# Kernel optimization log

Measured on AMD Instinct MI355X. Metric: run time of the kernel, lower is better.

Reference implementation:

```python
import jax, jax.numpy as jnp
import numpy as np

B_, L_, D_ = 2, 4096, 1024
E_ = 2
DI = E_ * D_            # 2048
H_ = 16
HD_ = DI // H_          # 128
N_ = 128
K_ = 4                  # d_conv
CS_ = 256               # SSD chunk size
MC_ = 256               # Hebbian memory chunk size
ALPHA = 0.5             # memory_alpha (== write_alpha default)


def _silu(x):
    return x * jax.nn.sigmoid(x)


def _rmsnorm(x, w, eps=1e-6):
    return x * jax.lax.rsqrt(jnp.mean(x * x, axis=-1, keepdims=True) + eps) * w


def setup_inputs() -> dict:
    key = jax.random.key(0)
    ks = jax.random.split(key, 8)
    proj_dim = 2 * DI + 2 * H_ * N_ + H_
    n = lambda k, sh, sc: jax.random.normal(k, sh, jnp.float32) * sc
    return {
        "x": n(ks[0], (B_, L_, D_), 1.0),
        "norm_w": jnp.ones((D_,), jnp.float32),
        "w_in": n(ks[1], (proj_dim, D_), 0.02),
        "conv_w": n(ks[2], (DI, K_), 0.2),
        "conv_b": jnp.zeros((DI,), jnp.float32),
        "A_log": jnp.log(2.0 * jnp.ones((H_,), jnp.float32)),
        "dt_bias": jnp.zeros((H_,), jnp.float32),
        "D_skip": jnp.ones((DI,), jnp.float32),
        "w_out": n(ks[3], (D_, DI), 0.02),
        "w_write": n(ks[4], (D_, D_), 0.02),
        "w_read": n(ks[5], (D_, D_), 0.02),
        "decay": jnp.float32(4.6),
    }


def _forward(x, norm_w, w_in, conv_w, conv_b, A_log, dt_bias, D_skip,
             w_out, w_write, w_read, decay):
    B, L, D = x.shape
    residual = x
    xn = _rmsnorm(x, norm_w)

    # ---- SSDBlock ----
    proj = xn @ w_in.T  # (B,L,2*DI+2*H*N+H)
    val = proj[..., :DI]
    gate = proj[..., DI:2 * DI]
    Bp = proj[..., 2 * DI:2 * DI + H_ * N_].reshape(B, L, H_, N_)
    Cp = proj[..., 2 * DI + H_ * N_:2 * DI + 2 * H_ * N_].reshape(B, L, H_, N_)
    dt = jax.nn.softplus(proj[..., -H_:] + dt_bias)  # (B,L,H)

    # causal depthwise conv1d (kernel K_, groups=DI)
    vp = jnp.pad(val, ((0, 0), (K_ - 1, 0), (0, 0)))
    val = sum(conv_w[:, k] * vp[:, k:k + L, :] for k in range(K_)) + conv_b
    val = _silu(val).reshape(B, L, H_, HD_)

    ld = dt * (-jnp.exp(A_log))  # log decay (B,L,H)

    nc = L // CS_
    to_chunks = lambda a: jnp.moveaxis(a.reshape(B, nc, CS_, *a.shape[2:]), 1, 0)
    tril = jnp.tril(jnp.ones((CS_, CS_), bool))
    Dv = D_skip.reshape(1, H_, 1, HD_)

    def ssd_chunk(h, inp):
        v_c, b_c, c_c, ld_c = inp  # (B,CS,H,HD), (B,CS,H,N), (B,CS,H,N), (B,CS,H)
        cum = jnp.cumsum(ld_c, axis=1)            # (B,CS,H)
        cum_h = jnp.transpose(cum, (0, 2, 1))     # (B,H,CS)
        dd = cum_h[:, :, :, None] - cum_h[:, :, None, :]
        Lmat = jnp.where(tril, jnp.exp(dd), 0.0)
        M = jnp.einsum('blhn,bmhn->bhlm', c_c, b_c) * Lmat
        v_h = jnp.transpose(v_c, (0, 2, 1, 3))    # (B,H,CS,HD)
        Y = M @ v_h
        Y = Y + jnp.einsum('blhn,bhdn,blh->bhld', c_c, h, jnp.exp(cum))
        Y = Y + Dv * v_h
        h = jnp.exp(cum[:, -1])[:, :, None, None] * h + \
            jnp.einsum('blhd,blhn,blh->bhdn', v_c, b_c, jnp.exp(cum[:, -1:, :] - cum))
        return h, Y

    h0 = jnp.zeros((B, H_, HD_, N_), jnp.float32)
    _, Ys = jax.lax.scan(ssd_chunk, h0,
                         (to_chunks(val), to_chunks(Bp), to_chunks(Cp), to_chunks(ld)))
    # (nc,B,H,CS,HD) -> (B,L,DI)
    Y = jnp.transpose(Ys, (1, 0, 3, 2, 4)).reshape(B, L, DI)
    out = (Y * _silu(gate)) @ w_out.T  # (B,L,D)

    # ---- Hebbian memory (chunkwise) ----
    gamma = jax.nn.sigmoid(decay)
    lg = jnp.log(gamma)
    v = out @ w_write.T
    wk = jnp.pad(out[:, :-1], ((0, 0), (1, 0), (0, 0)))  # shifted write keys
    p = jnp.arange(MC_)
    diffs = jnp.maximum(p[:, None] - 1 - p[None, :], 0).astype(jnp.float32)
    causal = (p[:, None] > p[None, :]).astype(jnp.float32)
    Mmem = jnp.exp(diffs * lg) * causal
    gp = gamma ** p                    # read decay by position in chunk
    gw = gamma ** (MC_ - 1 - p)        # write decay to end of chunk
    nm = L // MC_
    tom = lambda a: jnp.moveaxis(a.reshape(B, nm, MC_, D), 1, 0)

    def mem_chunk(W, inp):
        rk_c, wk_c, v_c = inp  # (B,MC,D)
        inter = jnp.einsum('bde,bte->btd', W, rk_c) * gp[None, :, None]
        S = jnp.einsum('bie,bje->bij', rk_c, wk_c)
        intra = (S * Mmem) @ v_c
        W = gamma ** MC_ * W + jnp.einsum('btd,bte->bde', v_c * gw[None, :, None], wk_c)
        return W, inter + intra

    W0 = jnp.zeros((B, D, D), jnp.float32)
    _, reads = jax.lax.scan(mem_chunk, W0, (tom(out), tom(wk), tom(v)))
    reads = jnp.moveaxis(reads, 0, 1).reshape(B, L, D)
    out = out + ALPHA * (reads @ w_read.T)
    return residual + out


def reference(x, norm_w, w_in, conv_w, conv_b, A_log, dt_bias, D_skip,
              w_out, w_write, w_read, decay):
    return _forward(x, norm_w, w_in, conv_w, conv_b, A_log, dt_bias, D_skip,
                    w_out, w_write, w_read, decay)
```

## Files before the change

kernel.cpp:

```cpp
#include <hip/hip_runtime.h>
#include <hip/hip_bf16.h>

typedef __hip_bfloat16 bf16;
typedef __attribute__((ext_vector_type(8))) short short8;
typedef __attribute__((ext_vector_type(4))) float floatx4;
typedef __attribute__((ext_vector_type(16))) float floatx16;

#define B_ 2
#define L_ 4096
#define D_ 1024
#define DI_ 2048
#define H_ 16
#define HD_ 128
#define N_ 128
#define CS_ 256
#define MC_ 256
#define NC_ 16
#define PROJ_ 8208

__device__ __forceinline__ float bf2f(short s) {
    return __uint_as_float(((unsigned)(unsigned short)s) << 16);
}
__device__ __forceinline__ short f2bf(float f) {
    __hip_bfloat16 h = __float2bfloat16(f);
    return *(short*)&h;
}

__device__ __forceinline__ void gl_lds16(const void* g, void* s) {
    __builtin_amdgcn_global_load_lds(
        (const __attribute__((address_space(1))) void*)g,
        (__attribute__((address_space(3))) void*)s, 16, 0, 0);
}

struct GemmP {
    const bf16* A; const bf16* Bt;
    float* C; bf16* CB; bf16* CB2; bf16* CB3;
    const float* add0; const float* add1; const bf16* add0b; const float* scr;
    long lda, ldb, ldc;
    int M, N, K, zinner, tri;
    long a_zo, a_zi, b_zo, b_zi, c_zo, c_zi;
};

template<int EPI>
__global__ __launch_bounds__(256, 2) void gemm_bt(GemmP p)
{
    int NT = gridDim.x, MT = gridDim.y;
    long T = (long)NT * MT * gridDim.z;
    long flat = ((long)blockIdx.z * MT + blockIdx.y) * NT + blockIdx.x;
    int xcd = (int)(flat & 7);
    long q = flat >> 3;
    long Tq = T >> 3; int Tr = (int)(T & 7);
    long tile = (long)xcd * Tq + (long)(xcd < Tr ? xcd : Tr) + q;
    long per_z = (long)NT * MT;
    int z = (int)(tile / per_z);
    int t2 = (int)(tile - (long)z * per_z);
    int FG = NT >> 3;
    int g, width, within;
    if (t2 < FG * MT * 8) { g = t2 / (MT * 8); width = 8; within = t2 - g * MT * 8; }
    else                  { g = FG; width = NT - FG * 8; within = t2 - FG * MT * 8; }
    int m_outer = within / (8 * width);
    int hb = MT - m_outer * 8; if (hb > 8) hb = 8;
    int inner = within - m_outer * 8 * width;
    int n_in = inner / hb, m_in = inner - n_in * hb;
    int m0 = (m_outer * 8 + m_in) * 128;
    int n0 = (g * 8 + n_in) * 128;

    int zo = z / p.zinner, zi = z % p.zinner;
    const bf16* A  = p.A  + (long)zo * p.a_zo + (long)zi * p.a_zi;
    const bf16* Bt = p.Bt + (long)zo * p.b_zo + (long)zi * p.b_zi;
    long coff = (long)zo * p.c_zo + (long)zi * p.c_zi;

    int tid = threadIdx.x;
    int lane = tid & 63, wave = tid >> 6;
    int wm = (wave >> 1) * 64, wn = (wave & 1) * 64;
    int ln31 = lane & 31, hi = lane >> 5;

    if (p.tri == 1 && n0 >= m0 + 128) {
        if (EPI == 3) {
#pragma unroll
            for (int i = 0; i < 2; i++)
#pragma unroll
                for (int j = 0; j < 2; j++)
#pragma unroll
                    for (int r = 0; r < 16; r++) {
                        int gm = m0 + wm + i * 32 + (r & 3) + 8 * (r >> 2) + 4 * hi;
                        int gn = n0 + wn + j * 32 + ln31;
                        if (gm < p.M && gn < p.N)
                            p.CB[coff + (long)gm * p.ldc + gn] = __float2bfloat16(0.f);
                    }
        }
        return;
    }
    int Keff = (p.tri == 2) ? (m0 + 128 < p.K ? m0 + 128 : p.K) : p.K;

    __shared__ __align__(16) bf16 As[128 * 64];
    __shared__ __align__(16) bf16 Bs[128 * 64];

    floatx16 acc[2][2];
#pragma unroll
    for (int i = 0; i < 2; i++)
#pragma unroll
        for (int j = 0; j < 2; j++)
#pragma unroll
            for (int r = 0; r < 16; r++) acc[i][j][r] = 0.f;

    int lrow = lane >> 3;
    int lc = ((lane & 7) ^ lrow) * 8;
    int wrow = wave * 32;
    int rx = lane & 7;

    for (int k0 = 0; k0 < Keff; k0 += 64) {
#pragma unroll
        for (int t = 0; t < 4; t++) {
            int row = wrow + t * 8 + lrow;
            gl_lds16(A + (long)(m0 + row) * p.lda + k0 + lc, &As[(wrow + t * 8) * 64]);
            int bn = n0 + row; if (bn > p.N - 1) bn = p.N - 1;
            gl_lds16(Bt + (long)bn * p.ldb + k0 + lc, &Bs[(wrow + t * 8) * 64]);
        }
        __syncthreads();
#pragma unroll
        for (int ks = 0; ks < 64; ks += 16) {
            int lb = (ks >> 3) + hi;
            int po = ((lb ^ rx) << 3);
            short8 af[2], bq[2];
#pragma unroll
            for (int i = 0; i < 2; i++)
                af[i] = *(const short8*)&As[(wm + i * 32 + ln31) * 64 + po];
#pragma unroll
            for (int j = 0; j < 2; j++)
                bq[j] = *(const short8*)&Bs[(wn + j * 32 + ln31) * 64 + po];
#pragma unroll
            for (int i = 0; i < 2; i++)
#pragma unroll
                for (int j = 0; j < 2; j++)
                    acc[i][j] = __builtin_amdgcn_mfma_f32_32x32x16_bf16(af[i], bq[j], acc[i][j], 0, 0, 0);
        }
        __syncthreads();
    }

#pragma unroll
    for (int i = 0; i < 2; i++) {
#pragma unroll
        for (int j = 0; j < 2; j++) {
#pragma unroll
            for (int r = 0; r < 16; r++) {
                int gm = m0 + wm + i * 32 + (r & 3) + 8 * (r >> 2) + 4 * hi;
                int gn = n0 + wn + j * 32 + ln31;
                if (gm >= p.M || gn >= p.N) continue;
                float a = acc[i][j][r];
                if (EPI == 0) {
                    p.C[coff + (long)gm * p.ldc + gn] = a;
                } else if (EPI == 2) {
                    if (gn < 2048)      p.CB [(long)gm * 2048 + gn]          = __float2bfloat16(a);
                    else if (gn < 4096) p.CB2[(long)gm * 2048 + (gn - 2048)] = __float2bfloat16(a);
                    else if (gn < 8192) p.CB3[(long)gm * 4096 + (gn - 4096)] = __float2bfloat16(a);
                    else                p.C  [(long)gm * 16   + (gn - 8192)] = a;
                } else if (EPI == 3) {
                    float lg = p.scr[1];
                    float v = (gm > gn) ? a * __expf((float)(gm - 1 - gn) * lg) : 0.f;
                    p.CB[coff + (long)gm * p.ldc + gn] = __float2bfloat16(v);
                } else if (EPI == 4) {
                    long ix = coff + (long)gm * p.ldc + gn;
                    float t = a * p.scr[16 + gm] + __bfloat162float(p.add0b[ix]);
                    p.CB[ix] = __float2bfloat16(t);
                } else if (EPI == 6) {
                    p.CB[coff + (long)gm * p.ldc + gn] = __float2bfloat16(a);
                } else if (EPI == 7) {
                    long ix = (long)gm * p.ldc + gn;
                    p.C[ix] = p.add0[ix] + __bfloat162float(p.add0b[ix]) + 0.5f * a;
                } else if (EPI == 8) {
                    long ix = (long)gm * p.ldc + gn;
                    bf16 v = __float2bfloat16(a);
                    p.CB[ix] = v;
                    int l = gm & (L_ - 1);
                    if (l != L_ - 1) p.CB2[ix + p.ldc] = v;
                    if (l == 0) p.CB2[ix] = __float2bfloat16(0.f);
                }
            }
        }
    }
}

__global__ void k_gamma(const float* decay, float* scr)
{
    int t = threadIdx.x;
    float g = 1.f / (1.f + expf(-decay[0]));
    float lg = logf(g);
    if (t == 0) { scr[0] = g; scr[1] = lg; scr[2] = expf(256.f * lg); }
    scr[16 + t]  = expf(lg * (float)t);
    scr[272 + t] = expf(lg * (float)(255 - t));
}

__global__ void k_f2ball(const float* __restrict__ s0, bf16* __restrict__ d0, long n0,
                         const float* __restrict__ s1, bf16* __restrict__ d1, long n1,
                         const float* __restrict__ s2, bf16* __restrict__ d2, long n2,
                         const float* __restrict__ s3, bf16* __restrict__ d3, long n3)
{
    long i = (long)blockIdx.x * 256 + threadIdx.x;
    const float* s; bf16* d; long rel = i;
    if (rel < n0) { s = s0; d = d0; }
    else { rel -= n0;
        if (rel < n1) { s = s1; d = d1; }
        else { rel -= n1;
            if (rel < n2) { s = s2; d = d2; }
            else { rel -= n2; if (rel >= n3) return; s = s3; d = d3; }
        }
    }
    float4 v = ((const float4*)s)[rel];
    bf16* o = d + rel * 4;
    o[0] = __float2bfloat16(v.x); o[1] = __float2bfloat16(v.y);
    o[2] = __float2bfloat16(v.z); o[3] = __float2bfloat16(v.w);
}

__global__ __launch_bounds__(256) void k_rmsnorm(const float* __restrict__ x,
                                                 const float* __restrict__ w,
                                                 bf16* __restrict__ o)
{
    int row = blockIdx.x, t = threadIdx.x;
    float4 xv = ((const float4*)(x + (long)row * D_))[t];
    float s = xv.x*xv.x + xv.y*xv.y + xv.z*xv.z + xv.w*xv.w;
#pragma unroll
    for (int m = 32; m > 0; m >>= 1) s += __shfl_xor(s, m, 64);
    __shared__ float ps[4];
    if ((t & 63) == 0) ps[t >> 6] = s;
    __syncthreads();
    s = ps[0] + ps[1] + ps[2] + ps[3];
    float r = rsqrtf(s * (1.f / (float)D_) + 1e-6f);
    float4 wv = ((const float4*)w)[t];
    bf16* orow = o + (long)row * D_ + t * 4;
    orow[0] = __float2bfloat16(xv.x * r * wv.x);
    orow[1] = __float2bfloat16(xv.y * r * wv.y);
    orow[2] = __float2bfloat16(xv.z * r * wv.z);
    orow[3] = __float2bfloat16(xv.w * r * wv.w);
}

__global__ __launch_bounds__(256) void k_cum(const float* __restrict__ dtr,
                                             const float* __restrict__ dt_bias,
                                             const float* __restrict__ A_log,
                                             float* __restrict__ cum_g,
                                             float* __restrict__ cumlast)
{
    int bid = blockIdx.x;
    int h = bid & 15, c = (bid >> 4) & 15, b = bid >> 8;
    long rowbase = (long)b * L_ + c * CS_;
    int tid = threadIdx.x;
    __shared__ float cum_s[256];
    float d = dtr[(rowbase + tid) * H_ + h] + dt_bias[h];
    float sp = (d > 20.f) ? d : log1pf(__expf(d));
    cum_s[tid] = -__expf(A_log[h]) * sp;
    __syncthreads();
    for (int off = 1; off < 256; off <<= 1) {
        float add = (tid >= off) ? cum_s[tid - off] : 0.f;
        __syncthreads();
        cum_s[tid] += add;
        __syncthreads();
    }
    cum_g[(rowbase + tid) * H_ + h] = cum_s[tid];
    if (tid == 255) cumlast[bid] = cum_s[255];
}

__global__ void k_vtc(const bf16* __restrict__ val_b, const float* __restrict__ cw,
                      const float* __restrict__ cb, bf16* __restrict__ vT)
{
    __shared__ bf16 tile[35][33];
    int b = blockIdx.z;
    int r0 = blockIdx.x * 32, c0 = blockIdx.y * 32;
    int tid = threadIdx.x;
    for (int idx = tid; idx < 35 * 32; idx += 256) {
        int row = idx >> 5, ch = idx & 31;
        int gl = r0 - 3 + row;
        bf16 v = __float2bfloat16(0.f);
        if (gl >= 0 && gl < L_) v = val_b[((long)b * L_ + gl) * 2048 + c0 + ch];
        tile[row][ch] = v;
    }
    __syncthreads();
    int tx = tid & 31, ty = tid >> 5;
    int l = r0 + tx;
    for (int i = 0; i < 32; i += 8) {
        int ch = c0 + ty + i;
        float4 cwv = ((const float4*)cw)[ch];
        float acc = cb[ch]
                  + cwv.x * __bfloat162float(tile[tx][ty + i])
                  + cwv.y * __bfloat162float(tile[tx + 1][ty + i])
                  + cwv.z * __bfloat162float(tile[tx + 2][ty + i])
                  + cwv.w * __bfloat162float(tile[tx + 3][ty + i]);
        float s = acc / (1.f + __expf(-acc));
        vT[((long)b * 2048 + ch) * L_ + l] = __float2bfloat16(s);
    }
}

__global__ void k_bt(const bf16* __restrict__ bc, bf16* __restrict__ BT)
{
    __shared__ bf16 tile[32][33];
    int b = blockIdx.z;
    int r0 = blockIdx.x * 32, c0 = blockIdx.y * 32;
    int tx = threadIdx.x & 31, ty = threadIdx.x >> 5;
    for (int i = 0; i < 32; i += 8)
        tile[ty + i][tx] = bc[((long)b * L_ + r0 + ty + i) * 4096 + c0 + tx];
    __syncthreads();
    int l = r0 + tx;
    for (int i = 0; i < 32; i += 8) {
        int col = c0 + ty + i;
        BT[((long)b * 2048 + col) * L_ + l] = tile[tx][ty + i];
    }
}

__global__ __launch_bounds__(256, 2) void k_ssd_u2(
    const bf16* __restrict__ vT, const bf16* __restrict__ BT,
    const float* __restrict__ cum_g, const float* __restrict__ cumlast,
    bf16* __restrict__ U)
{
    int bid = blockIdx.x;
    int h = bid & 15, c = (bid >> 4) & 15, b = bid >> 8;
    long rowbase = (long)b * L_ + c * CS_;
    int tid = threadIdx.x;
    __shared__ float w_s[256];
    w_s[tid] = __expf(cumlast[bid] - cum_g[(rowbase + tid) * H_ + h]);
    __syncthreads();
    int lane = tid & 63, wave = tid >> 6;
    int r16 = lane & 15, q8 = (lane >> 4) * 8, rq = (lane >> 4) * 4;
    int d0 = (wave >> 1) * 64, n0 = (wave & 1) * 64;
    const bf16* vb = vT + ((long)b * 2048 + h * 128) * L_ + c * 256;
    const bf16* bb = BT + ((long)b * 2048 + h * 128) * L_ + c * 256;
    floatx4 zero4 = {0.f, 0.f, 0.f, 0.f};
    floatx4 acc[4][4];
#pragma unroll
    for (int i = 0; i < 4; i++)
#pragma unroll
        for (int j = 0; j < 4; j++) acc[i][j] = zero4;
#pragma unroll 2
    for (int ks = 0; ks < 8; ks++) {
        float wv[8];
#pragma unroll
        for (int j = 0; j < 8; j++) wv[j] = w_s[ks * 32 + q8 + j];
        short8 af[4], bq[4];
#pragma unroll
        for (int i = 0; i < 4; i++) {
            short8 raw = *(const short8*)(vb + (long)(d0 + i * 16 + r16) * L_ + ks * 32 + q8);
#pragma unroll
            for (int j = 0; j < 8; j++) {
                float f = bf2f(raw[j]) * wv[j];
                raw[j] = (short)(__float_as_uint(f) >> 16);
            }
            af[i] = raw;
        }
#pragma unroll
        for (int j = 0; j < 4; j++)
            bq[j] = *(const short8*)(bb + (long)(n0 + j * 16 + r16) * L_ + ks * 32 + q8);
#pragma unroll
        for (int i = 0; i < 4; i++)
#pragma unroll
            for (int j = 0; j < 4; j++)
                acc[i][j] = __builtin_amdgcn_mfma_f32_16x16x32_bf16(af[i], bq[j], acc[i][j], 0, 0, 0);
    }
    bf16* up = U + (((long)c * B_ + b) * H_ + h) * 16384;
#pragma unroll
    for (int i = 0; i < 4; i++)
#pragma unroll
        for (int j = 0; j < 4; j++)
#pragma unroll
            for (int r = 0; r < 4; r++)
                up[(d0 + i * 16 + rq + r) * 128 + (n0 + j * 16 + r16)] = __float2bfloat16(acc[i][j][r]);
}

__global__ void k_ssd2(const bf16* __restrict__ U, const float* __restrict__ cumlast,
                       bf16* __restrict__ hst)
{
    const long tot = (long)B_ * H_ * HD_ * N_;
    long idx = ((long)blockIdx.x * 256 + threadIdx.x) * 8;
    if (idx >= tot) return;
    int bh = (int)(idx >> 14);
    int b = bh >> 4, h = bh & 15;
    float hv[8];
#pragma unroll
    for (int j = 0; j < 8; j++) hv[j] = 0.f;
    for (int c = 0; c < NC_; c++) {
        float ef = __expf(cumlast[b * 256 + c * 16 + h]);
        short8 u = *(const short8*)(U + c * tot + idx);
        short8 o;
#pragma unroll
        for (int j = 0; j < 8; j++) {
            o[j] = f2bf(hv[j]);
            hv[j] = ef * hv[j] + bf2f(u[j]);
        }
        *(short8*)(hst + c * tot + idx) = o;
    }
}

__global__ __launch_bounds__(256, 2) void k_ssd_y(
    const bf16* __restrict__ bc_b, const bf16* __restrict__ vT,
    const bf16* __restrict__ hst, const float* __restrict__ cum_g,
    const float* __restrict__ Dskip, const bf16* __restrict__ gate_b,
    bf16* __restrict__ yg)
{
    int bid = blockIdx.x;
    int h = bid & 15, c = (bid >> 4) & 15, b = bid >> 8;
    long rowbase = (long)b * L_ + c * CS_;
    int tid = threadIdx.x, lane = tid & 63, wave = tid >> 6;
    int r16 = lane & 15, q8 = (lane >> 4) * 8, rq = (lane >> 4) * 4;
    int wt = (wave >> 1) * 32, wmS = (wave & 1) * 32, wd = (wave & 1) * 64;

    __shared__ float cum_s[256];
    __shared__ __align__(16) bf16 Ss[64][72];

    cum_s[tid] = cum_g[(rowbase + tid) * H_ + h];
    __syncthreads();

    const bf16* Cb  = bc_b + rowbase * 4096 + 2048 + h * 128;
    const bf16* Bb  = bc_b + rowbase * 4096 + h * 128;
    const bf16* vTb = vT + ((long)b * 2048 + h * 128) * L_ + c * 256;
    const bf16* hp  = hst + (((long)c * B_ + b) * H_ + h) * 16384;

    floatx4 zero4 = {0.f, 0.f, 0.f, 0.f};

    for (int tt = 0; tt < 4; tt++) {
        int tbase = tt * 64;
        short8 caf[2][4];
#pragma unroll
        for (int i = 0; i < 2; i++)
#pragma unroll
            for (int ks = 0; ks < 4; ks++)
                caf[i][ks] = *(const short8*)(Cb + (long)(tbase + wt + i * 16 + r16) * 4096 + ks * 32 + q8);

        floatx4 yacc[2][4];
#pragma unroll
        for (int i = 0; i < 2; i++)
#pragma unroll
            for (int j = 0; j < 4; j++) yacc[i][j] = zero4;
#pragma unroll
        for (int ks = 0; ks < 4; ks++)
#pragma unroll
            for (int j = 0; j < 4; j++) {
                short8 hq = *(const short8*)(hp + (long)(wd + j * 16 + r16) * 128 + ks * 32 + q8);
#pragma unroll
                for (int i = 0; i < 2; i++)
                    yacc[i][j] = __builtin_amdgcn_mfma_f32_16x16x32_bf16(caf[i][ks], hq, yacc[i][j], 0, 0, 0);
            }
        float texp[2][4];
#pragma unroll
        for (int i = 0; i < 2; i++)
#pragma unroll
            for (int r = 0; r < 4; r++)
                texp[i][r] = __expf(cum_s[tbase + wt + i * 16 + rq + r]);
#pragma unroll
        for (int i = 0; i < 2; i++)
#pragma unroll
            for (int j = 0; j < 4; j++)
#pragma unroll
                for (int r = 0; r < 4; r++) yacc[i][j][r] *= texp[i][r];

        for (int mt = 0; mt <= tt; mt++) {
            int mbase = mt * 64;
            floatx4 sacc[2][2];
#pragma unroll
            for (int i = 0; i < 2; i++)
#pragma unroll
                for (int j = 0; j < 2; j++) sacc[i][j] = zero4;
#pragma unroll
            for (int ks = 0; ks < 4; ks++) {
                short8 bq[2];
#pragma unroll
                for (int j = 0; j < 2; j++)
                    bq[j] = *(const short8*)(Bb + (long)(mbase + wmS + j * 16 + r16) * 4096 + ks * 32 + q8);
#pragma unroll
                for (int i = 0; i < 2; i++)
#pragma unroll
                    for (int j = 0; j < 2; j++)
                        sacc[i][j] = __builtin_amdgcn_mfma_f32_16x16x32_bf16(caf[i][ks], bq[j], sacc[i][j], 0, 0, 0);
            }
            __syncthreads();
#pragma unroll
            for (int i = 0; i < 2; i++)
#pragma unroll
                for (int r = 0; r < 4; r++) {
                    int trow = wt + i * 16 + rq + r;
                    float ct = cum_s[tbase + trow];
#pragma unroll
                    for (int j = 0; j < 2; j++) {
                        int mcol = mbase + wmS + j * 16 + r16;
                        float val = (mcol <= tbase + trow) ? sacc[i][j][r] * __expf(ct - cum_s[mcol]) : 0.f;
                        Ss[trow][wmS + j * 16 + r16] = __float2bfloat16(val);
                    }
                }
            __syncthreads();
#pragma unroll
            for (int ks = 0; ks < 2; ks++) {
                short8 saf[2];
#pragma unroll
                for (int i = 0; i < 2; i++)
                    saf[i] = *(const short8*)&Ss[wt + i * 16 + r16][ks * 32 + q8];
#pragma unroll
                for (int j = 0; j < 4; j++) {
                    short8 vq = *(const short8*)(vTb + (long)(wd + j * 16 + r16) * L_ + mbase + ks * 32 + q8);
#pragma unroll
                    for (int i = 0; i < 2; i++)
                        yacc[i][j] = __builtin_amdgcn_mfma_f32_16x16x32_bf16(saf[i], vq, yacc[i][j], 0, 0, 0);
                }
            }
        }
#pragma unroll
        for (int i = 0; i < 2; i++)
#pragma unroll
            for (int r = 0; r < 4; r++) {
                int t = tbase + wt + i * 16 + rq + r;
                long grow = (rowbase + t) * 2048 + h * 128;
#pragma unroll
                for (int j = 0; j < 4; j++) {
                    int d = wd + j * 16 + r16;
                    float vv = __bfloat162float(vTb[(long)d * L_ + t]);
                    float y = yacc[i][j][r] + Dskip[h * 128 + d] * vv;
                    float g = __bfloat162float(gate_b[grow + d]);
                    float sg = g / (1.f + __expf(-g));
                    yg[grow + d] = __float2bfloat16(y * sg);
                }
            }
    }
}

__global__ void k_trans2(const bf16* __restrict__ vbuf, const bf16* __restrict__ outg,
                         const float* __restrict__ scr,
                         bf16* __restrict__ vTm, bf16* __restrict__ wkgT)
{
    __shared__ bf16 tv[32][33];
    __shared__ bf16 tw[32][33];
    int b = blockIdx.z;
    const bf16* srcv = vbuf + (long)b * L_ * D_;
    const bf16* srco = outg + (long)b * L_ * D_;
    int r0 = blockIdx.x * 32, c0 = blockIdx.y * 32;
    int tx = threadIdx.x & 31, ty = threadIdx.x >> 5;
    for (int i = 0; i < 32; i += 8) {
        int rr = r0 + ty + i;
        tv[ty + i][tx] = srcv[(long)rr * D_ + c0 + tx];
        float g = scr[272 + (rr & 255)];
        float w = (rr == 0) ? 0.f : __bfloat162float(srco[(long)(rr - 1) * D_ + c0 + tx]) * g;
        tw[ty + i][tx] = __float2bfloat16(w);
    }
    __syncthreads();
    bf16* dv = vTm + (long)b * D_ * L_;
    bf16* dw = wkgT + (long)b * D_ * L_;
    for (int i = 0; i < 32; i += 8) {
        long o = (long)(c0 + ty + i) * L_ + r0 + tx;
        dv[o] = tv[tx][ty + i];
        dw[o] = tw[tx][ty + i];
    }
}

__global__ void k_m2(bf16* __restrict__ UwW, const float* __restrict__ scr)
{
    const long tot = (long)B_ * D_ * D_;
    long idx = ((long)blockIdx.x * 256 + threadIdx.x) * 8;
    if (idx >= tot) return;
    float gMC = scr[2];
    float w[8];
#pragma unroll
    for (int j = 0; j < 8; j++) w[j] = 0.f;
    for (int c = 0; c < NC_; c++) {
        short8 u = *(const short8*)(UwW + c * tot + idx);
        short8 o;
#pragma unroll
        for (int j = 0; j < 8; j++) {
            o[j] = f2bf(w[j]);
            w[j] = gMC * w[j] + bf2f(u[j]);
        }
        *(short8*)(UwW + c * tot + idx) = o;
    }
}

static inline int cdiv_i(long a, long b) { return (int)((a + b - 1) / b); }

static void run_gemm(hipStream_t st, int epi, const bf16* A, const bf16* Bt,
                     float* C, bf16* CB, bf16* CB2, bf16* CB3,
                     const float* add0, const float* add1, const bf16* add0b,
                     const float* scr, int M, int N, int K,
                     long lda, long ldb, long ldc, int nbatch, int zinner,
                     long a_zo, long a_zi, long b_zo, long b_zi, long c_zo, long c_zi,
                     int tri = 0)
{
    GemmP p;
    p.A = A; p.Bt = Bt; p.C = C; p.CB = CB; p.CB2 = CB2; p.CB3 = CB3;
    p.add0 = add0; p.add1 = add1; p.add0b = add0b; p.scr = scr;
    p.lda = lda; p.ldb = ldb; p.ldc = ldc;
    p.M = M; p.N = N; p.K = K; p.zinner = zinner; p.tri = tri;
    p.a_zo = a_zo; p.a_zi = a_zi; p.b_zo = b_zo; p.b_zi = b_zi; p.c_zo = c_zo; p.c_zi = c_zi;
    dim3 g(cdiv_i(N, 128), cdiv_i(M, 128), nbatch);
    dim3 b(256);
    switch (epi) {
        case 0: gemm_bt<0><<<g, b, 0, st>>>(p); break;
        case 2: gemm_bt<2><<<g, b, 0, st>>>(p); break;
        case 3: gemm_bt<3><<<g, b, 0, st>>>(p); break;
        case 4: gemm_bt<4><<<g, b, 0, st>>>(p); break;
        case 6: gemm_bt<6><<<g, b, 0, st>>>(p); break;
        case 7: gemm_bt<7><<<g, b, 0, st>>>(p); break;
        case 8: gemm_bt<8><<<g, b, 0, st>>>(p); break;
    }
}

extern "C" void kernel_launch(void* const* d_in, const int* in_sizes, int n_in,
                              void* d_out, int out_size, void* d_ws, size_t ws_size,
                              hipStream_t stream)
{
    const float* x       = (const float*)d_in[0];
    const float* norm_w  = (const float*)d_in[1];
    const float* w_in    = (const float*)d_in[2];
    const float* conv_w  = (const float*)d_in[3];
    const float* conv_b  = (const float*)d_in[4];
    const float* A_log   = (const float*)d_in[5];
    const float* dt_bias = (const float*)d_in[6];
    const float* D_skip  = (const float*)d_in[7];
    const float* w_out   = (const float*)d_in[8];
    const float* w_write = (const float*)d_in[9];
    const float* w_read  = (const float*)d_in[10];
    const float* decay   = (const float*)d_in[11];
    float* outp = (float*)d_out;

    const size_t SZ_SCR  = 4096;
    const size_t SZ_DT   = (size_t)B_ * L_ * H_ * 4;
    const size_t SZ_CUML = 2048;
    const size_t SZ_WOUT = (size_t)D_ * DI_ * 2;
    const size_t SZ_WSML = (size_t)D_ * D_ * 2;
    const size_t SZ_R1   = (size_t)B_ * L_ * 2048 * 2;
    const size_t SZ_R2   = SZ_R1;
    const size_t SZ_R3   = (size_t)B_ * L_ * 4096 * 2;
    const size_t SZ_R4   = (size_t)B_ * L_ * D_ * 2 + (size_t)PROJ_ * D_ * 2;
    const size_t SZ_R5   = (size_t)B_ * L_ * 2048 * 4;

    size_t o = 0;
    auto take = [&](size_t sz) { size_t r = o; o += (sz + 255) & ~(size_t)255; return r; };
    const size_t O_SCR = take(SZ_SCR);
    const size_t O_DT  = take(SZ_DT);
    const size_t O_LD  = take(SZ_DT);
    const size_t O_CUM = take(SZ_DT);
    const size_t O_CL  = take(SZ_CUML);
    const size_t O_WO  = take(SZ_WOUT);
    const size_t O_WW  = take(SZ_WSML);
    const size_t O_WR  = take(SZ_WSML);
    const size_t O_R1  = take(SZ_R1);
    const size_t O_R2  = take(SZ_R2);
    const size_t O_R3  = take(SZ_R3);
    const size_t O_R4  = take(SZ_R4);
    const size_t O_R5  = take(SZ_R5);
    const size_t NEED = o;
    if (ws_size < NEED) return;
    (void)O_LD;

    char* ws = (char*)d_ws;
    float* scr     = (float*)(ws + O_SCR);
    float* dt_raw  = (float*)(ws + O_DT);
    float* cum_g   = (float*)(ws + O_CUM);
    float* cumlast = (float*)(ws + O_CL);
    bf16*  w_out_b   = (bf16*)(ws + O_WO);
    bf16*  w_write_b = (bf16*)(ws + O_WW);
    bf16*  w_read_b  = (bf16*)(ws + O_WR);

    bf16*  val_b   = (bf16*)(ws + O_R1);
    bf16*  yg_b    = (bf16*)(ws + O_R1);
    bf16*  hst_b   = (bf16*)(ws + O_R1 + (size_t)B_ * L_ * D_ * 2);
    bf16*  Sm_b    = (bf16*)(ws + O_R1);
    bf16*  intra_b = (bf16*)(ws + O_R1 + (size_t)NC_ * B_ * MC_ * MC_ * 2);
    bf16*  gate_b  = (bf16*)(ws + O_R2);
    bf16*  out_b   = (bf16*)(ws + O_R2);
    bf16*  wk_b    = (bf16*)(ws + O_R2 + (size_t)B_ * L_ * D_ * 2);
    bf16*  reads_b = wk_b;
    bf16*  bc_b    = (bf16*)(ws + O_R3);
    bf16*  UwW     = (bf16*)(ws + O_R3);
    bf16*  xn_b    = (bf16*)(ws + O_R4);
    bf16*  w_in_b  = (bf16*)(ws + O_R4 + (size_t)B_ * L_ * D_ * 2);
    bf16*  U_ssd   = (bf16*)(ws + O_R4);
    bf16*  vT_g    = (bf16*)(ws + O_R5);
    bf16*  BT_g    = (bf16*)(ws + O_R5 + (size_t)B_ * L_ * 2048 * 2);
    bf16*  vbuf_b  = (bf16*)(ws + O_R5);
    bf16*  vTm     = (bf16*)(ws + O_R5 + (size_t)B_ * L_ * D_ * 4);
    bf16*  wkgT    = (bf16*)(ws + O_R5 + (size_t)B_ * L_ * D_ * 4 + (size_t)B_ * L_ * D_ * 2);

    k_gamma<<<1, 256, 0, stream>>>(decay, scr);
    {
        long n0 = (long)PROJ_ * D_ / 4, n1 = (long)D_ * DI_ / 4;
        long n2 = (long)D_ * D_ / 4,   n3 = n2;
        k_f2ball<<<cdiv_i(n0 + n1 + n2 + n3, 256), 256, 0, stream>>>(
            w_in, w_in_b, n0, w_out, w_out_b, n1, w_write, w_write_b, n2, w_read, w_read_b, n3);
    }
    k_rmsnorm<<<B_ * L_, 256, 0, stream>>>(x, norm_w, xn_b);
    run_gemm(stream, 2, xn_b, w_in_b, dt_raw, val_b, gate_b, bc_b, nullptr, nullptr, nullptr, nullptr,
             B_ * L_, PROJ_, D_, D_, D_, 0, 1, 1, 0, 0, 0, 0, 0, 0);
    k_cum<<<B_ * NC_ * H_, 256, 0, stream>>>(dt_raw, dt_bias, A_log, cum_g, cumlast);
    k_vtc<<<dim3(L_ / 32, DI_ / 32, B_), 256, 0, stream>>>(val_b, conv_w, conv_b, vT_g);
    k_bt<<<dim3(L_ / 32, DI_ / 32, B_), 256, 0, stream>>>(bc_b, BT_g);
    k_ssd_u2<<<B_ * NC_ * H_, 256, 0, stream>>>(vT_g, BT_g, cum_g, cumlast, U_ssd);
    k_ssd2<<<cdiv_i((long)B_ * H_ * HD_ * N_ / 8, 256), 256, 0, stream>>>(U_ssd, cumlast, hst_b);
    k_ssd_y<<<B_ * NC_ * H_, 256, 0, stream>>>(bc_b, vT_g, hst_b, cum_g, D_skip, gate_b, yg_b);
    run_gemm(stream, 8, yg_b, w_out_b, nullptr, out_b, wk_b, nullptr, nullptr, nullptr, nullptr, nullptr,
             B_ * L_, D_, DI_, DI_, DI_, D_, 1, 1, 0, 0, 0, 0, 0, 0);
    run_gemm(stream, 6, out_b, w_write_b, nullptr, vbuf_b, nullptr, nullptr, nullptr, nullptr, nullptr, nullptr,
             B_ * L_, D_, D_, D_, D_, D_, 1, 1, 0, 0, 0, 0, 0, 0);
    k_trans2<<<dim3(L_ / 32, D_ / 32, B_), 256, 0, stream>>>(vbuf_b, out_b, scr, vTm, wkgT);
    run_gemm(stream, 6, vTm, wkgT, nullptr, UwW, nullptr, nullptr, nullptr, nullptr, nullptr, nullptr,
             D_, D_, MC_, L_, L_, D_, B_ * NC_, NC_,
             (long)D_ * L_, MC_, (long)D_ * L_, MC_, (long)D_ * D_, (long)B_ * D_ * D_);
    k_m2<<<cdiv_i((long)B_ * D_ * D_ / 8, 256), 256, 0, stream>>>(UwW, scr);
    run_gemm(stream, 3, out_b, wk_b, nullptr, Sm_b, nullptr, nullptr, nullptr, nullptr, nullptr, scr,
             MC_, MC_, D_, D_, D_, MC_, B_ * NC_, NC_,
             (long)L_ * D_, (long)MC_ * D_, (long)L_ * D_, (long)MC_ * D_,
             (long)MC_ * MC_, (long)B_ * MC_ * MC_, 1);
    run_gemm(stream, 6, Sm_b, vTm, nullptr, intra_b, nullptr, nullptr, nullptr, nullptr, nullptr, nullptr,
             MC_, D_, MC_, MC_, L_, D_, B_ * NC_, NC_,
             (long)MC_ * MC_, (long)B_ * MC_ * MC_, (long)D_ * L_, MC_,
             (long)L_ * D_, (long)MC_ * D_, 2);
    run_gemm(stream, 4, out_b, UwW, nullptr, reads_b, nullptr, nullptr, nullptr, nullptr, intra_b, scr,
             MC_, D_, D_, D_, D_, D_, B_ * NC_, NC_,
             (long)L_ * D_, (long)MC_ * D_, (long)D_ * D_, (long)B_ * D_ * D_,
             (long)L_ * D_, (long)MC_ * D_);
    run_gemm(stream, 7, reads_b, w_read_b, outp, nullptr, nullptr, nullptr, x, nullptr, out_b, nullptr,
             B_ * L_, D_, D_, D_, D_, D_, 1, 1, 0, 0, 0, 0, 0, 0);
}
```

Before: 756.2 us.

## Fuse transposed stores into GEMM epilogues and drop separate transpose kernels

The input-projection GEMM epilogue now stages the accumulator tile in shared memory and writes the val and B projections already transposed (channel-major) to global memory. This removes the k_bt transpose kernel and lets the conv/SiLU kernel become a simple vectorized row pass. The write-projection GEMM likewise emits the transposed value matrix directly through a new epilogue, so the follow-up transpose kernel only has to handle the gated write keys. The cost is an extra LDS round trip and barrier in those epilogues, plus a shared buffer reused between the main loop and the epilogue.

```diff
diff --git a/kernel.cpp b/kernel.cpp
--- a/kernel.cpp
+++ b/kernel.cpp
@@ -34,7 +34,7 @@
 
 struct GemmP {
     const bf16* A; const bf16* Bt;
-    float* C; bf16* CB; bf16* CB2; bf16* CB3;
+    float* C; bf16* CB; bf16* CB2; bf16* CB3; bf16* CB4;
     const float* add0; const float* add1; const bf16* add0b; const float* scr;
     long lda, ldb, ldc;
     int M, N, K, zinner, tri;
@@ -75,6 +75,10 @@
     int wm = (wave >> 1) * 64, wn = (wave & 1) * 64;
     int ln31 = lane & 31, hi = lane >> 5;
 
+    __shared__ __align__(16) bf16 Sh[2 * 128 * 64];
+    bf16* As = Sh;
+    bf16* Bs = Sh + 128 * 64;
+
     if (p.tri == 1 && n0 >= m0 + 128) {
         if (EPI == 3) {
 #pragma unroll
@@ -93,9 +97,6 @@
     }
     int Keff = (p.tri == 2) ? (m0 + 128 < p.K ? m0 + 128 : p.K) : p.K;
 
-    __shared__ __align__(16) bf16 As[128 * 64];
-    __shared__ __align__(16) bf16 Bs[128 * 64];
-
     floatx16 acc[2][2];
 #pragma unroll
     for (int i = 0; i < 2; i++)
@@ -138,44 +139,78 @@
         __syncthreads();
     }
 
-#pragma unroll
-    for (int i = 0; i < 2; i++) {
-#pragma unroll
-        for (int j = 0; j < 2; j++) {
-#pragma unroll
-            for (int r = 0; r < 16; r++) {
-                int gm = m0 + wm + i * 32 + (r & 3) + 8 * (r >> 2) + 4 * hi;
-                int gn = n0 + wn + j * 32 + ln31;
-                if (gm >= p.M || gn >= p.N) continue;
-                float a = acc[i][j][r];
-                if (EPI == 0) {
-                    p.C[coff + (long)gm * p.ldc + gn] = a;
-                } else if (EPI == 2) {
-                    if (gn < 2048)      p.CB [(long)gm * 2048 + gn]          = __float2bfloat16(a);
-                    else if (gn < 4096) p.CB2[(long)gm * 2048 + (gn - 2048)] = __float2bfloat16(a);
-                    else if (gn < 8192) p.CB3[(long)gm * 4096 + (gn - 4096)] = __float2bfloat16(a);
-                    else                p.C  [(long)gm * 16   + (gn - 8192)] = a;
-                } else if (EPI == 3) {
-                    float lg = p.scr[1];
-                    float v = (gm > gn) ? a * __expf((float)(gm - 1 - gn) * lg) : 0.f;
-                    p.CB[coff + (long)gm * p.ldc + gn] = __float2bfloat16(v);
-                } else if (EPI == 4) {
-                    long ix = coff + (long)gm * p.ldc + gn;
-                    float t = a * p.scr[16 + gm] + __bfloat162float(p.add0b[ix]);
-                    p.CB[ix] = __float2bfloat16(t);
-                } else if (EPI == 6) {
-                    p.CB[coff + (long)gm * p.ldc + gn] = __float2bfloat16(a);
-                } else if (EPI == 7) {
-                    long ix = (long)gm * p.ldc + gn;
-                    p.C[ix] = p.add0[ix] + __bfloat162float(p.add0b[ix]) + 0.5f * a;
-                } else if (EPI == 8) {
-                    long ix = (long)gm * p.ldc + gn;
-                    bf16 v = __float2bfloat16(a);
-                    p.CB[ix] = v;
-                    int l = gm & (L_ - 1);
-                    if (l != L_ - 1) p.CB2[ix + p.ldc] = v;
-                    if (l == 0) p.CB2[ix] = __float2bfloat16(0.f);
+    if (EPI != 9) {
+#pragma unroll
+        for (int i = 0; i < 2; i++) {
+#pragma unroll
+            for (int j = 0; j < 2; j++) {
+#pragma unroll
+                for (int r = 0; r < 16; r++) {
+                    int gm = m0 + wm + i * 32 + (r & 3) + 8 * (r >> 2) + 4 * hi;
+                    int gn = n0 + wn + j * 32 + ln31;
+                    if (gm >= p.M || gn >= p.N) continue;
+                    float a = acc[i][j][r];
+                    if (EPI == 0) {
+                        p.C[coff + (long)gm * p.ldc + gn] = a;
+                    } else if (EPI == 2) {
+                        if (gn >= 8192)     p.C  [(long)gm * 16   + (gn - 8192)] = a;
+                        else if (gn >= 4096) p.CB3[(long)gm * 4096 + (gn - 4096)] = __float2bfloat16(a);
+                        else if (gn >= 2048) p.CB2[(long)gm * 2048 + (gn - 2048)] = __float2bfloat16(a);
+                    } else if (EPI == 3) {
+                        float lg = p.scr[1];
+                        float v = (gm > gn) ? a * __expf((float)(gm - 1 - gn) * lg) : 0.f;
+                        p.CB[coff + (long)gm * p.ldc + gn] = __float2bfloat16(v);
+                    } else if (EPI == 4) {
+                        long ix = coff + (long)gm * p.ldc + gn;
+                        float t = a * p.scr[16 + gm] + __bfloat162float(p.add0b[ix]);
+                        p.CB[ix] = __float2bfloat16(t);
+                    } else if (EPI == 6) {
+                        p.CB[coff + (long)gm * p.ldc + gn] = __float2bfloat16(a);
+                    } else if (EPI == 7) {
+                        long ix = (long)gm * p.ldc + gn;
+                        p.C[ix] = p.add0[ix] + __bfloat162float(p.add0b[ix]) + 0.5f * a;
+                    } else if (EPI == 8) {
+                        long ix = (long)gm * p.ldc + gn;
+                        bf16 v = __float2bfloat16(a);
+                        p.CB[ix] = v;
+                        int l = gm & (L_ - 1);
+                        if (l != L_ - 1) p.CB2[ix + p.ldc] = v;
+                        if (l == 0) p.CB2[ix] = __float2bfloat16(0.f);
+                    }
                 }
+            }
+        }
+    }
+
+    if (EPI == 2 || EPI == 9) {
+        bool doT = (EPI == 9) || (n0 < 2048) || (n0 >= 4096 && n0 < 6144);
+        if (doT) {
+#pragma unroll
+            for (int i = 0; i < 2; i++)
+#pragma unroll
+                for (int j = 0; j < 2; j++)
+#pragma unroll
+                    for (int r = 0; r < 16; r++) {
+                        int lr = wm + i * 32 + (r & 3) + 8 * (r >> 2) + 4 * hi;
+                        int lcn = wn + j * 32 + ln31;
+                        Sh[lr * 128 + lcn] = __float2bfloat16(acc[i][j][r]);
+                    }
+            __syncthreads();
+            int bloc = m0 >> 12;
+            int l0 = m0 & (L_ - 1);
+            int dl = tid & 127, lh = tid >> 7;
+            bf16* dst;
+            if (EPI == 9)        dst = p.CB  + ((long)bloc * D_   + n0          + dl) * L_ + l0;
+            else if (n0 < 2048)  dst = p.CB  + ((long)bloc * 2048 + n0          + dl) * L_ + l0;
+            else                 dst = p.CB4 + ((long)bloc * 2048 + (n0 - 4096) + dl) * L_ + l0;
+            const short* shs = (const short*)Sh;
+#pragma unroll
+            for (int s = 0; s < 8; s++) {
+                int ls = lh * 64 + s * 8;
+                short8 v;
+#pragma unroll
+                for (int u = 0; u < 8; u++) v[u] = shs[(ls + u) * 128 + dl];
+                *(short8*)(dst + ls) = v;
             }
         }
     }
@@ -259,50 +294,32 @@
     if (tid == 255) cumlast[bid] = cum_s[255];
 }
 
-__global__ void k_vtc(const bf16* __restrict__ val_b, const float* __restrict__ cw,
-                      const float* __restrict__ cb, bf16* __restrict__ vT)
-{
-    __shared__ bf16 tile[35][33];
-    int b = blockIdx.z;
-    int r0 = blockIdx.x * 32, c0 = blockIdx.y * 32;
-    int tid = threadIdx.x;
-    for (int idx = tid; idx < 35 * 32; idx += 256) {
-        int row = idx >> 5, ch = idx & 31;
-        int gl = r0 - 3 + row;
-        bf16 v = __float2bfloat16(0.f);
-        if (gl >= 0 && gl < L_) v = val_b[((long)b * L_ + gl) * 2048 + c0 + ch];
-        tile[row][ch] = v;
-    }
-    __syncthreads();
-    int tx = tid & 31, ty = tid >> 5;
-    int l = r0 + tx;
-    for (int i = 0; i < 32; i += 8) {
-        int ch = c0 + ty + i;
-        float4 cwv = ((const float4*)cw)[ch];
-        float acc = cb[ch]
-                  + cwv.x * __bfloat162float(tile[tx][ty + i])
-                  + cwv.y * __bfloat162float(tile[tx + 1][ty + i])
-                  + cwv.z * __bfloat162float(tile[tx + 2][ty + i])
-                  + cwv.w * __bfloat162float(tile[tx + 3][ty + i]);
-        float s = acc / (1.f + __expf(-acc));
-        vT[((long)b * 2048 + ch) * L_ + l] = __float2bfloat16(s);
-    }
-}
-
-__global__ void k_bt(const bf16* __restrict__ bc, bf16* __restrict__ BT)
-{
-    __shared__ bf16 tile[32][33];
-    int b = blockIdx.z;
-    int r0 = blockIdx.x * 32, c0 = blockIdx.y * 32;
-    int tx = threadIdx.x & 31, ty = threadIdx.x >> 5;
-    for (int i = 0; i < 32; i += 8)
-        tile[ty + i][tx] = bc[((long)b * L_ + r0 + ty + i) * 4096 + c0 + tx];
-    __syncthreads();
-    int l = r0 + tx;
-    for (int i = 0; i < 32; i += 8) {
-        int col = c0 + ty + i;
-        BT[((long)b * 2048 + col) * L_ + l] = tile[tx][ty + i];
-    }
+__global__ void k_vtc2(const bf16* __restrict__ valT, const float* __restrict__ cw,
+                       const float* __restrict__ cb, bf16* __restrict__ vT)
+{
+    int row = blockIdx.y;
+    int ch = row & 2047;
+    long base = (long)row * L_;
+    int l0 = blockIdx.x * 2048 + threadIdx.x * 8;
+    short8 cur = *(const short8*)(valT + base + l0);
+    short8 prev;
+#pragma unroll
+    for (int u = 0; u < 8; u++) prev[u] = 0;
+    if (l0 >= 8) prev = *(const short8*)(valT + base + l0 - 8);
+    float4 cwv = ((const float4*)cw)[ch];
+    float bias = cb[ch];
+    float v[11];
+    v[0] = bf2f(prev[5]); v[1] = bf2f(prev[6]); v[2] = bf2f(prev[7]);
+#pragma unroll
+    for (int u = 0; u < 8; u++) v[3 + u] = bf2f(cur[u]);
+    short8 o;
+#pragma unroll
+    for (int u = 0; u < 8; u++) {
+        float a = bias + cwv.x * v[u] + cwv.y * v[u + 1] + cwv.z * v[u + 2] + cwv.w * v[u + 3];
+        float s = a / (1.f + __expf(-a));
+        o[u] = f2bf(s);
+    }
+    *(short8*)(vT + base + l0) = o;
 }
 
 __global__ __launch_bounds__(256, 2) void k_ssd_u2(
@@ -517,32 +534,23 @@
     }
 }
 
-__global__ void k_trans2(const bf16* __restrict__ vbuf, const bf16* __restrict__ outg,
-                         const float* __restrict__ scr,
-                         bf16* __restrict__ vTm, bf16* __restrict__ wkgT)
-{
-    __shared__ bf16 tv[32][33];
-    __shared__ bf16 tw[32][33];
+__global__ void k_trans_wkg(const bf16* __restrict__ outg, const float* __restrict__ scr,
+                            bf16* __restrict__ dstg)
+{
+    __shared__ float t[32][33];
     int b = blockIdx.z;
-    const bf16* srcv = vbuf + (long)b * L_ * D_;
-    const bf16* srco = outg + (long)b * L_ * D_;
+    const bf16* src = outg + (long)b * L_ * D_;
+    bf16* dst = dstg + (long)b * D_ * L_;
     int r0 = blockIdx.x * 32, c0 = blockIdx.y * 32;
     int tx = threadIdx.x & 31, ty = threadIdx.x >> 5;
     for (int i = 0; i < 32; i += 8) {
         int rr = r0 + ty + i;
-        tv[ty + i][tx] = srcv[(long)rr * D_ + c0 + tx];
         float g = scr[272 + (rr & 255)];
-        float w = (rr == 0) ? 0.f : __bfloat162float(srco[(long)(rr - 1) * D_ + c0 + tx]) * g;
-        tw[ty + i][tx] = __float2bfloat16(w);
+        t[ty + i][tx] = (rr == 0) ? 0.f : __bfloat162float(src[(long)(rr - 1) * D_ + c0 + tx]) * g;
     }
     __syncthreads();
-    bf16* dv = vTm + (long)b * D_ * L_;
-    bf16* dw = wkgT + (long)b * D_ * L_;
-    for (int i = 0; i < 32; i += 8) {
-        long o = (long)(c0 + ty + i) * L_ + r0 + tx;
-        dv[o] = tv[tx][ty + i];
-        dw[o] = tw[tx][ty + i];
-    }
+    for (int i = 0; i < 32; i += 8)
+        dst[(long)(c0 + ty + i) * L_ + r0 + tx] = __float2bfloat16(t[tx][ty + i]);
 }
 
 __global__ void k_m2(bf16* __restrict__ UwW, const float* __restrict__ scr)
@@ -574,10 +582,10 @@
                      const float* scr, int M, int N, int K,
                      long lda, long ldb, long ldc, int nbatch, int zinner,
                      long a_zo, long a_zi, long b_zo, long b_zi, long c_zo, long c_zi,
-                     int tri = 0)
+                     int tri = 0, bf16* CB4 = nullptr)
 {
     GemmP p;
-    p.A = A; p.Bt = Bt; p.C = C; p.CB = CB; p.CB2 = CB2; p.CB3 = CB3;
+    p.A = A; p.Bt = Bt; p.C = C; p.CB = CB; p.CB2 = CB2; p.CB3 = CB3; p.CB4 = CB4;
     p.add0 = add0; p.add1 = add1; p.add0b = add0b; p.scr = scr;
     p.lda = lda; p.ldb = ldb; p.ldc = ldc;
     p.M = M; p.N = N; p.K = K; p.zinner = zinner; p.tri = tri;
@@ -592,6 +600,7 @@
         case 6: gemm_bt<6><<<g, b, 0, st>>>(p); break;
         case 7: gemm_bt<7><<<g, b, 0, st>>>(p); break;
         case 8: gemm_bt<8><<<g, b, 0, st>>>(p); break;
+        case 9: gemm_bt<9><<<g, b, 0, st>>>(p); break;
     }
 }
 
@@ -652,7 +661,7 @@
     bf16*  w_write_b = (bf16*)(ws + O_WW);
     bf16*  w_read_b  = (bf16*)(ws + O_WR);
 
-    bf16*  val_b   = (bf16*)(ws + O_R1);
+    bf16*  valT    = (bf16*)(ws + O_R1);
     bf16*  yg_b    = (bf16*)(ws + O_R1);
     bf16*  hst_b   = (bf16*)(ws + O_R1 + (size_t)B_ * L_ * D_ * 2);
     bf16*  Sm_b    = (bf16*)(ws + O_R1);
@@ -668,7 +677,6 @@
     bf16*  U_ssd   = (bf16*)(ws + O_R4);
     bf16*  vT_g    = (bf16*)(ws + O_R5);
     bf16*  BT_g    = (bf16*)(ws + O_R5 + (size_t)B_ * L_ * 2048 * 2);
-    bf16*  vbuf_b  = (bf16*)(ws + O_R5);
     bf16*  vTm     = (bf16*)(ws + O_R5 + (size_t)B_ * L_ * D_ * 4);
     bf16*  wkgT    = (bf16*)(ws + O_R5 + (size_t)B_ * L_ * D_ * 4 + (size_t)B_ * L_ * D_ * 2);
 
@@ -680,19 +688,18 @@
             w_in, w_in_b, n0, w_out, w_out_b, n1, w_write, w_write_b, n2, w_read, w_read_b, n3);
     }
     k_rmsnorm<<<B_ * L_, 256, 0, stream>>>(x, norm_w, xn_b);
-    run_gemm(stream, 2, xn_b, w_in_b, dt_raw, val_b, gate_b, bc_b, nullptr, nullptr, nullptr, nullptr,
-             B_ * L_, PROJ_, D_, D_, D_, 0, 1, 1, 0, 0, 0, 0, 0, 0);
+    run_gemm(stream, 2, xn_b, w_in_b, dt_raw, valT, gate_b, bc_b, nullptr, nullptr, nullptr, nullptr,
+             B_ * L_, PROJ_, D_, D_, D_, 0, 1, 1, 0, 0, 0, 0, 0, 0, 0, BT_g);
     k_cum<<<B_ * NC_ * H_, 256, 0, stream>>>(dt_raw, dt_bias, A_log, cum_g, cumlast);
-    k_vtc<<<dim3(L_ / 32, DI_ / 32, B_), 256, 0, stream>>>(val_b, conv_w, conv_b, vT_g);
-    k_bt<<<dim3(L_ / 32, DI_ / 32, B_), 256, 0, stream>>>(bc_b, BT_g);
+    k_vtc2<<<dim3(L_ / 2048, B_ * DI_), 256, 0, stream>>>(valT, conv_w, conv_b, vT_g);
     k_ssd_u2<<<B_ * NC_ * H_, 256, 0, stream>>>(vT_g, BT_g, cum_g, cumlast, U_ssd);
     k_ssd2<<<cdiv_i((long)B_ * H_ * HD_ * N_ / 8, 256), 256, 0, stream>>>(U_ssd, cumlast, hst_b);
     k_ssd_y<<<B_ * NC_ * H_, 256, 0, stream>>>(bc_b, vT_g, hst_b, cum_g, D_skip, gate_b, yg_b);
     run_gemm(stream, 8, yg_b, w_out_b, nullptr, out_b, wk_b, nullptr, nullptr, nullptr, nullptr, nullptr,
              B_ * L_, D_, DI_, DI_, DI_, D_, 1, 1, 0, 0, 0, 0, 0, 0);
-    run_gemm(stream, 6, out_b, w_write_b, nullptr, vbuf_b, nullptr, nullptr, nullptr, nullptr, nullptr, nullptr,
+    run_gemm(stream, 9, out_b, w_write_b, nullptr, vTm, nullptr, nullptr, nullptr, nullptr, nullptr, nullptr,
              B_ * L_, D_, D_, D_, D_, D_, 1, 1, 0, 0, 0, 0, 0, 0);
-    k_trans2<<<dim3(L_ / 32, D_ / 32, B_), 256, 0, stream>>>(vbuf_b, out_b, scr, vTm, wkgT);
+    k_trans_wkg<<<dim3(L_ / 32, D_ / 32, B_), 256, 0, stream>>>(out_b, scr, wkgT);
     run_gemm(stream, 6, vTm, wkgT, nullptr, UwW, nullptr, nullptr, nullptr, nullptr, nullptr, nullptr,
              D_, D_, MC_, L_, L_, D_, B_ * NC_, NC_,
              (long)D_ * L_, MC_, (long)D_ * L_, MC_, (long)D_ * D_, (long)B_ * D_ * D_);
```

New measurement: 737.2 us. 1.03x faster.
